# Optimization experiments

Measured on AMD Instinct MI355X. Metric: run time of the kernel, lower is better.

Reference implementation:

```python
import jax, jax.numpy as jnp
import numpy as np
import math

N_ENT = 200000
N_USERS = 100000
N_FACTORS = 4
N_REL = 26
CH = 64
N_EDGES = 1000000
NNZ = 1000000
KG_HEADS = 2


def scatter_softmax(scores, seg, num_segments):
    # numerically-stable softmax over groups defined by seg (per-head softmax)
    m = jax.ops.segment_max(scores, seg, num_segments=num_segments)
    m = jnp.where(jnp.isfinite(m), m, 0.0)
    e = jnp.exp(scores - m[seg])
    d = jax.ops.segment_sum(e, seg, num_segments=num_segments)
    return e / d[seg]


def setup_inputs() -> dict:
    key = jax.random.key(0)
    ks = jax.random.split(key, 11)
    return {
        "entity_emb": jax.random.normal(ks[0], (N_ENT, CH), dtype=jnp.float32) * 0.1,
        "user_emb": jax.random.normal(ks[1], (N_USERS, CH), dtype=jnp.float32) * 0.1,
        "latent_emb": jax.random.normal(ks[2], (N_FACTORS, CH), dtype=jnp.float32) * 0.1,
        "edge_index": jax.random.randint(ks[3], (2, N_EDGES), 0, N_ENT),
        "edge_type": jax.random.randint(ks[4], (N_EDGES,), 1, N_REL),  # in [1, N_REL-1]
        "ui_rows": jax.random.randint(ks[5], (NNZ,), 0, N_USERS),
        "ui_cols": jax.random.randint(ks[6], (NNZ,), 0, N_ENT),
        "ui_vals": jax.random.uniform(ks[7], (NNZ,), dtype=jnp.float32),
        "weight": jax.random.normal(ks[8], (N_REL - 1, CH), dtype=jnp.float32) * 0.1,
        "disen_weight_att": jax.random.normal(ks[9], (N_FACTORS, N_REL - 1), dtype=jnp.float32) * 0.1,
        "kg_W_r": jax.random.normal(ks[10], (CH, CH), dtype=jnp.float32) * (1.0 / math.sqrt(CH)),
    }


def reference(entity_emb, user_emb, latent_emb, edge_index, edge_type,
              ui_rows, ui_cols, ui_vals, weight, disen_weight_att, kg_W_r):
    head, tail = edge_index[0], edge_index[1]
    d_k = CH // KG_HEADS

    # --- Invariant_Capture.relation_aware_att ---
    rel_emb = weight[edge_type - 1]            # [E, C] gather
    h_emb = entity_emb[head]                   # [E, C] gather
    q = (h_emb @ kg_W_r).reshape(-1, KG_HEADS, d_k)
    k = (rel_emb @ kg_W_r).reshape(-1, KG_HEADS, d_k)
    score_r = ((q * k).sum(-1) / math.sqrt(d_k)).mean(-1)   # [E]
    rel_attn = scatter_softmax(score_r, head, N_ENT)

    # --- Invariant_Capture.kg_inv_capture ---
    t_emb = entity_emb[tail]                   # [E, C] gather
    r_emb = rel_emb * rel_attn[:, None]
    # bmm(cat(h,r), cat(t,r)^T) == h.t + r.r per edge
    score_trip = (h_emb * t_emb).sum(-1) + (r_emb * r_emb).sum(-1)
    kg_mask = scatter_softmax(score_trip, head, N_ENT)       # invariant_mask [E]

    # --- Aggregator: KG scatter-mean with invariant mask ---
    neigh = t_emb * rel_emb * kg_mask[:, None]               # [E, C]
    sums = jax.ops.segment_sum(neigh, head, num_segments=N_ENT)
    cnt = jax.ops.segment_sum(jnp.ones((neigh.shape[0],), dtype=neigh.dtype), head, num_segments=N_ENT)
    entity_agg = sums / jnp.maximum(cnt, 1.0)[:, None]       # scatter_mean

    # --- Aggregator: user side ---
    score = jax.nn.softmax(user_emb @ latent_emb.T, axis=1)  # [U, F]
    user_agg = jax.ops.segment_sum(entity_emb[ui_cols] * ui_vals[:, None], ui_rows, num_segments=N_USERS)
    disen_weight = jax.nn.softmax(disen_weight_att, axis=-1) @ weight  # [F, C]
    # (expand(U,F,C) * score[:,:,None]).sum(1) == score @ disen_weight
    user_agg = user_agg * (score @ disen_weight) + user_agg

    return jnp.concatenate([entity_agg, user_agg], axis=0)   # [N_ENT+N_USERS, C]
```

## Files before the change

### kernel.cpp

```cpp
#include <hip/hip_runtime.h>
#include <math.h>

#define N_ENT 200000
#define N_USERS 100000
#define NKEY 300000
#define N_FACTORS 4
#define NREL1 25
#define CH 64
#define N_EDGES 1000000
#define NNZ 1000000
#define NREC 2000000
#define BSHIFT 11
#define BKEYS 2048
#define NBUCKET 147
#define TILE 2048
#define CAP 24576
#define NCONVB ((N_ENT * 8 + 1023) / 1024)

#define SCORE_SCALE 0.08838834764831845f
#define INV_Q14 6.103888176768602e-05f

__device__ __forceinline__ float red8(float d) {
    d += __shfl_xor(d, 1);
    d += __shfl_xor(d, 2);
    d += __shfl_xor(d, 4);
    return d;
}
__device__ __forceinline__ float dot4(float4 a, float4 b) {
    return a.x * b.x + a.y * b.y + a.z * b.z + a.w * b.w;
}
__device__ __forceinline__ unsigned short f2bf(float f) {
    unsigned u = __float_as_uint(f);
    u += 0x7FFFu + ((u >> 16) & 1u);
    return (unsigned short)(u >> 16);
}
__device__ __forceinline__ float bf2f(unsigned short u) {
    return __uint_as_float(((unsigned)u) << 16);
}
__device__ __forceinline__ float4 bf4lo(uint4 t) {
    return make_float4(__uint_as_float(t.x << 16), __uint_as_float(t.x & 0xFFFF0000u),
                       __uint_as_float(t.y << 16), __uint_as_float(t.y & 0xFFFF0000u));
}
__device__ __forceinline__ float4 bf4hi(uint4 t) {
    return make_float4(__uint_as_float(t.z << 16), __uint_as_float(t.z & 0xFFFF0000u),
                       __uint_as_float(t.w << 16), __uint_as_float(t.w & 0xFFFF0000u));
}

__global__ void precompute_k(const float* __restrict__ W,
                             const float* __restrict__ weight,
                             const float* __restrict__ datt,
                             float* __restrict__ Mvec,
                             float* __restrict__ wnorm,
                             float* __restrict__ disen) {
    __shared__ float sW[64 * 64];
    __shared__ float sw[NREL1 * 64];
    __shared__ float sWWt[64 * 64];
    int tid = threadIdx.x;
    for (int i = tid; i < 64 * 64; i += 256) sW[i] = W[i];
    for (int i = tid; i < NREL1 * 64; i += 256) sw[i] = weight[i];
    __syncthreads();
    for (int e = tid; e < 64 * 64; e += 256) {
        int i = e >> 6, j = e & 63;
        float s = 0.f;
        for (int k = 0; k < 64; ++k) s += sW[i * 64 + k] * sW[j * 64 + k];
        sWWt[e] = s;
    }
    __syncthreads();
    for (int e = tid; e < NREL1 * 64; e += 256) {
        int r = e >> 6, i = e & 63;
        float s = 0.f;
        for (int j = 0; j < 64; ++j) s += sWWt[i * 64 + j] * sw[r * 64 + j];
        Mvec[e] = s;
    }
    for (int r = tid; r < NREL1; r += 256) {
        float s = 0.f;
        for (int j = 0; j < 64; ++j) { float v = sw[r * 64 + j]; s += v * v; }
        wnorm[r] = s;
    }
    for (int e = tid; e < N_FACTORS * 64; e += 256) {
        int f = e >> 6, c = e & 63;
        float m = -1e30f;
        for (int r = 0; r < NREL1; ++r) m = fmaxf(m, datt[f * NREL1 + r]);
        float ssum = 0.f, acc = 0.f;
        for (int r = 0; r < NREL1; ++r) {
            float p = expf(datt[f * NREL1 + r] - m);
            ssum += p;
            acc += p * sw[r * 64 + c];
        }
        disen[e] = acc / ssum;
    }
}

__global__ void binfill_k(const int* __restrict__ head, const int* __restrict__ tail,
                          const int* __restrict__ etype,
                          const int* __restrict__ rows, const int* __restrict__ cols,
                          const float* __restrict__ vals,
                          unsigned* __restrict__ gcur,
                          uint2* __restrict__ stg) {
    __shared__ unsigned hist[NBUCKET], gbase[NBUCKET];
    int tid = threadIdx.x;
    int tile0 = blockIdx.x * TILE;
    int tile_n = min(TILE, NREC - tile0);
    for (int b = tid; b < NBUCKET; b += 256) hist[b] = 0u;
    __syncthreads();
    unsigned key[8], pay[8], rank[8];
    for (int r = 0; r < 8; ++r) {
        int li = r * 256 + tid;
        key[r] = 0xFFFFFFFFu;
        if (li < tile_n) {
            int idx = tile0 + li;
            unsigned k, p;
            if (idx < N_EDGES) {
                k = (unsigned)head[idx];
                p = (unsigned)tail[idx] | ((unsigned)(etype[idx] - 1) << 18);
            } else {
                int j = idx - N_EDGES;
                k = (unsigned)(N_ENT + rows[j]);
                unsigned q = (unsigned)(vals[j] * 16383.f + 0.5f);
                p = (unsigned)cols[j] | (q << 18);
            }
            key[r] = k; pay[r] = p;
            rank[r] = atomicAdd(&hist[k >> BSHIFT], 1u);
        }
    }
    __syncthreads();
    if (tid < NBUCKET) {
        unsigned v = hist[tid];
        gbase[tid] = (unsigned)tid * CAP + (v ? atomicAdd(&gcur[tid], v) : 0u);
    }
    __syncthreads();
    for (int r = 0; r < 8; ++r) {
        if (key[r] != 0xFFFFFFFFu) {
            unsigned b = key[r] >> BSHIFT;
            unsigned dst = gbase[b] + rank[r];
            if (dst < (b + 1u) * CAP)
                stg[dst] = make_uint2(key[r], pay[r]);
        }
    }
}

__device__ __forceinline__
void place_bucket_dev(int b, int tid, const uint2* __restrict__ stg,
                      const unsigned* __restrict__ gcur,
                      unsigned* __restrict__ offs, unsigned* __restrict__ csr,
                      unsigned* shm) {
    unsigned c = (tid < NBUCKET) ? gcur[tid] : 0u;
    if (c > CAP) c = CAP;
    if (tid < 256) shm[tid] = c;
    __syncthreads();
    for (int o = 1; o < 256; o <<= 1) {
        unsigned t = (tid >= o && tid < 256) ? shm[tid - o] : 0u;
        __syncthreads();
        if (tid < 256) shm[tid] += t;
        __syncthreads();
    }
    if (tid == 0) {
        unsigned cb = gcur[b]; if (cb > CAP) cb = CAP;
        shm[3073] = cb;
        shm[3072] = shm[b] - cb;
        if (b == NBUCKET - 1) offs[NKEY] = shm[NBUCKET - 1];
    }
    __syncthreads();
    unsigned n = shm[3073], gb = shm[3072];
    const uint2* seg = stg + (size_t)b * CAP;
    unsigned* cnt = shm;
    unsigned* sc  = shm + 2048;
    cnt[tid * 2] = 0u; cnt[tid * 2 + 1] = 0u;
    __syncthreads();
    for (unsigned i = tid; i < n; i += 1024) {
        unsigned kk = seg[i].x - ((unsigned)b << BSHIFT);
        atomicAdd(&cnt[kk], 1u);
    }
    __syncthreads();
    unsigned c0 = cnt[tid * 2], c1 = cnt[tid * 2 + 1];
    unsigned tsum = c0 + c1;
    sc[tid] = tsum; __syncthreads();
    for (int o = 1; o < 1024; o <<= 1) {
        unsigned t = (tid >= o) ? sc[tid - o] : 0u;
        __syncthreads();
        sc[tid] += t;
        __syncthreads();
    }
    unsigned e0 = sc[tid] - tsum;
    unsigned e1 = e0 + c0;
    int k0 = (b << BSHIFT) + tid * 2;
    if (k0 < NKEY)     offs[k0]     = gb + e0;
    if (k0 + 1 < NKEY) offs[k0 + 1] = gb + e1;
    cnt[tid * 2] = e0; cnt[tid * 2 + 1] = e1;
    __syncthreads();
    for (unsigned i = tid; i < n; i += 1024) {
        uint2 rec = seg[i];
        unsigned kk = rec.x - ((unsigned)b << BSHIFT);
        unsigned pos = atomicAdd(&cnt[kk], 1u);
        csr[gb + pos] = rec.y;
    }
}

__device__ __forceinline__
void convE_dev(int cb, int tid, const float* __restrict__ ent,
               const float* __restrict__ Mvec,
               uint4* __restrict__ entb, unsigned short* __restrict__ E16,
               unsigned* shm) {
    float4* sM = (float4*)shm;
    for (int i = tid; i < NREL1 * 16; i += 1024) sM[i] = ((const float4*)Mvec)[i];
    __syncthreads();
    int idx = cb * 1024 + tid;
    int h = idx >> 3;
    int sub = tid & 7;
    if (h >= N_ENT) return;
    const float4* e4 = (const float4*)ent;
    float4 a = e4[h * 16 + sub * 2], b4 = e4[h * 16 + sub * 2 + 1];
    uint4 o;
    o.x = (unsigned)f2bf(a.x)  | ((unsigned)f2bf(a.y)  << 16);
    o.y = (unsigned)f2bf(a.z)  | ((unsigned)f2bf(a.w)  << 16);
    o.z = (unsigned)f2bf(b4.x) | ((unsigned)f2bf(b4.y) << 16);
    o.w = (unsigned)f2bf(b4.z) | ((unsigned)f2bf(b4.w) << 16);
    entb[h * 8 + sub] = o;
    for (int r = 0; r < NREL1; ++r) {
        float d = dot4(a, sM[r * 16 + sub * 2]) + dot4(b4, sM[r * 16 + sub * 2 + 1]);
        d = red8(d);
        if (sub == (r & 7)) E16[h * NREL1 + r] = f2bf(__expf(d * SCORE_SCALE));
    }
}

__global__ void binplace3_k(const uint2* __restrict__ stg,
                            const unsigned* __restrict__ gcur,
                            unsigned* __restrict__ offs,
                            unsigned* __restrict__ csr) {
    __shared__ __align__(16) unsigned shm[3074];
    place_bucket_dev(blockIdx.x, threadIdx.x, stg, gcur, offs, csr, shm);
}

__global__ void convE2_k(const float* __restrict__ ent,
                         const float* __restrict__ Mvec,
                         uint4* __restrict__ entb,
                         unsigned short* __restrict__ E16) {
    __shared__ __align__(16) unsigned shm[3074];
    convE_dev(blockIdx.x, threadIdx.x, ent, Mvec, entb, E16, shm);
}

__global__ void placeconv_k(const uint2* __restrict__ stg,
                            const unsigned* __restrict__ gcur,
                            unsigned* __restrict__ offs,
                            unsigned* __restrict__ csr,
                            const float* __restrict__ ent,
                            const float* __restrict__ Mvec,
                            uint4* __restrict__ entb,
                            unsigned short* __restrict__ E16) {
    __shared__ __align__(16) unsigned shm[3074];
    int b = blockIdx.x;
    if (b < NBUCKET)
        place_bucket_dev(b, threadIdx.x, stg, gcur, offs, csr, shm);
    else
        convE_dev(b - NBUCKET, threadIdx.x, ent, Mvec, entb, E16, shm);
}

template<bool FAST>
__global__ void gather8_k(const float* __restrict__ ent,
                          const uint4* __restrict__ entb,
                          const unsigned short* __restrict__ E16,
                          const float* __restrict__ weight,
                          const float* __restrict__ Mvec,
                          const float* __restrict__ wnorm,
                          const float* __restrict__ uemb,
                          const float* __restrict__ lat,
                          const float* __restrict__ disen,
                          const unsigned* __restrict__ offs,
                          const unsigned* __restrict__ csr,
                          float* __restrict__ out) {
    int gid = blockIdx.x * 256 + threadIdx.x;
    int key = gid >> 3;
    int sub = threadIdx.x & 7;
    if (key >= NKEY) return;
    unsigned beg = offs[key], end = offs[key + 1];
    const float4* e4 = (const float4*)ent;
    const float4* w4 = (const float4*)weight;
    float4* o4 = (float4*)out;
    const float4 z = make_float4(0.f, 0.f, 0.f, 0.f);

    if (key < N_ENT) {
        int h = key;
        if (beg == end) {
            o4[h * 16 + sub * 2] = z;
            o4[h * 16 + sub * 2 + 1] = z;
            return;
        }
        float4 hv0, hv1;
        if (FAST) {
            uint4 hb = entb[h * 8 + sub];
            hv0 = bf4lo(hb); hv1 = bf4hi(hb);
        } else {
            hv0 = e4[h * 16 + sub * 2]; hv1 = e4[h * 16 + sub * 2 + 1];
        }
        float dr = 0.f;
        if (FAST) {
            for (unsigned i = beg + sub; i < end; i += 8)
                dr += bf2f(E16[h * NREL1 + (csr[i] >> 18)]);
            dr = red8(dr);
        } else {
            for (unsigned i = beg; i < end; ++i) {
                int r = csr[i] >> 18;
                float d = dot4(hv0, ((const float4*)Mvec)[r * 16 + sub * 2]) +
                          dot4(hv1, ((const float4*)Mvec)[r * 16 + sub * 2 + 1]);
                dr += __expf(red8(d) * SCORE_SCALE);
            }
        }
        float inv_dr = 1.0f / dr;
        float4 a0 = z, a1 = z;
        float dt = 0.f;
        unsigned i = beg;
        for (; i + 2 <= end; i += 2) {
            unsigned p0 = csr[i], p1 = csr[i + 1];
            int t0 = p0 & 0x3FFFF, r0 = p0 >> 18;
            int t1 = p1 & 0x3FFFF, r1 = p1 >> 18;
            float4 tv00, tv01, tv10, tv11;
            if (FAST) {
                uint4 tb0 = entb[t0 * 8 + sub];
                uint4 tb1 = entb[t1 * 8 + sub];
                tv00 = bf4lo(tb0); tv01 = bf4hi(tb0);
                tv10 = bf4lo(tb1); tv11 = bf4hi(tb1);
            } else {
                tv00 = e4[t0 * 16 + sub * 2]; tv01 = e4[t0 * 16 + sub * 2 + 1];
                tv10 = e4[t1 * 16 + sub * 2]; tv11 = e4[t1 * 16 + sub * 2 + 1];
            }
            float d0 = red8(dot4(hv0, tv00) + dot4(hv1, tv01));
            float d1 = red8(dot4(hv0, tv10) + dot4(hv1, tv11));
            float er0, er1;
            if (FAST) {
                er0 = bf2f(E16[h * NREL1 + r0]);
                er1 = bf2f(E16[h * NREL1 + r1]);
            } else {
                float q0 = dot4(hv0, ((const float4*)Mvec)[r0 * 16 + sub * 2]) +
                           dot4(hv1, ((const float4*)Mvec)[r0 * 16 + sub * 2 + 1]);
                float q1 = dot4(hv0, ((const float4*)Mvec)[r1 * 16 + sub * 2]) +
                           dot4(hv1, ((const float4*)Mvec)[r1 * 16 + sub * 2 + 1]);
                er0 = __expf(red8(q0) * SCORE_SCALE);
                er1 = __expf(red8(q1) * SCORE_SCALE);
            }
            float ra0 = er0 * inv_dr, ra1 = er1 * inv_dr;
            float et0 = __expf(d0 + ra0 * ra0 * wnorm[r0]);
            float et1 = __expf(d1 + ra1 * ra1 * wnorm[r1]);
            dt += et0 + et1;
            float4 wv;
            wv = w4[r0 * 16 + sub * 2];
            a0.x += et0 * tv00.x * wv.x; a0.y += et0 * tv00.y * wv.y;
            a0.z += et0 * tv00.z * wv.z; a0.w += et0 * tv00.w * wv.w;
            wv = w4[r0 * 16 + sub * 2 + 1];
            a1.x += et0 * tv01.x * wv.x; a1.y += et0 * tv01.y * wv.y;
            a1.z += et0 * tv01.z * wv.z; a1.w += et0 * tv01.w * wv.w;
            wv = w4[r1 * 16 + sub * 2];
            a0.x += et1 * tv10.x * wv.x; a0.y += et1 * tv10.y * wv.y;
            a0.z += et1 * tv10.z * wv.z; a0.w += et1 * tv10.w * wv.w;
            wv = w4[r1 * 16 + sub * 2 + 1];
            a1.x += et1 * tv11.x * wv.x; a1.y += et1 * tv11.y * wv.y;
            a1.z += et1 * tv11.z * wv.z; a1.w += et1 * tv11.w * wv.w;
        }
        if (i < end) {
            unsigned p = csr[i];
            int t = p & 0x3FFFF, r = p >> 18;
            float4 tv0, tv1;
            if (FAST) {
                uint4 tb = entb[t * 8 + sub];
                tv0 = bf4lo(tb); tv1 = bf4hi(tb);
            } else {
                tv0 = e4[t * 16 + sub * 2]; tv1 = e4[t * 16 + sub * 2 + 1];
            }
            float d = red8(dot4(hv0, tv0) + dot4(hv1, tv1));
            float er;
            if (FAST) {
                er = bf2f(E16[h * NREL1 + r]);
            } else {
                float q = dot4(hv0, ((const float4*)Mvec)[r * 16 + sub * 2]) +
                          dot4(hv1, ((const float4*)Mvec)[r * 16 + sub * 2 + 1]);
                er = __expf(red8(q) * SCORE_SCALE);
            }
            float ra = er * inv_dr;
            float et = __expf(d + ra * ra * wnorm[r]);
            dt += et;
            float4 wv;
            wv = w4[r * 16 + sub * 2];
            a0.x += et * tv0.x * wv.x; a0.y += et * tv0.y * wv.y;
            a0.z += et * tv0.z * wv.z; a0.w += et * tv0.w * wv.w;
            wv = w4[r * 16 + sub * 2 + 1];
            a1.x += et * tv1.x * wv.x; a1.y += et * tv1.y * wv.y;
            a1.z += et * tv1.z * wv.z; a1.w += et * tv1.w * wv.w;
        }
        float inv = 1.0f / (dt * (float)(end - beg));
        a0.x *= inv; a0.y *= inv; a0.z *= inv; a0.w *= inv;
        a1.x *= inv; a1.y *= inv; a1.z *= inv; a1.w *= inv;
        o4[h * 16 + sub * 2] = a0;
        o4[h * 16 + sub * 2 + 1] = a1;
    } else {
        int u = key - N_ENT;
        float4 a0 = z, a1 = z;
        unsigned i = beg;
        for (; i + 2 <= end; i += 2) {
            unsigned p0 = csr[i], p1 = csr[i + 1];
            int c0 = p0 & 0x3FFFF, c1 = p1 & 0x3FFFF;
            float v0 = (float)(p0 >> 18) * INV_Q14;
            float v1 = (float)(p1 >> 18) * INV_Q14;
            float4 tv00, tv01, tv10, tv11;
            if (FAST) {
                uint4 tb0 = entb[c0 * 8 + sub];
                uint4 tb1 = entb[c1 * 8 + sub];
                tv00 = bf4lo(tb0); tv01 = bf4hi(tb0);
                tv10 = bf4lo(tb1); tv11 = bf4hi(tb1);
            } else {
                tv00 = e4[c0 * 16 + sub * 2]; tv01 = e4[c0 * 16 + sub * 2 + 1];
                tv10 = e4[c1 * 16 + sub * 2]; tv11 = e4[c1 * 16 + sub * 2 + 1];
            }
            a0.x += v0 * tv00.x + v1 * tv10.x; a0.y += v0 * tv00.y + v1 * tv10.y;
            a0.z += v0 * tv00.z + v1 * tv10.z; a0.w += v0 * tv00.w + v1 * tv10.w;
            a1.x += v0 * tv01.x + v1 * tv11.x; a1.y += v0 * tv01.y + v1 * tv11.y;
            a1.z += v0 * tv01.z + v1 * tv11.z; a1.w += v0 * tv01.w + v1 * tv11.w;
        }
        if (i < end) {
            unsigned p = csr[i];
            int c = p & 0x3FFFF;
            float v = (float)(p >> 18) * INV_Q14;
            float4 tv0, tv1;
            if (FAST) {
                uint4 tb = entb[c * 8 + sub];
                tv0 = bf4lo(tb); tv1 = bf4hi(tb);
            } else {
                tv0 = e4[c * 16 + sub * 2]; tv1 = e4[c * 16 + sub * 2 + 1];
            }
            a0.x += v * tv0.x; a0.y += v * tv0.y; a0.z += v * tv0.z; a0.w += v * tv0.w;
            a1.x += v * tv1.x; a1.y += v * tv1.y; a1.z += v * tv1.z; a1.w += v * tv1.w;
        }
        float4 uv0 = ((const float4*)uemb)[u * 16 + sub * 2];
        float4 uv1 = ((const float4*)uemb)[u * 16 + sub * 2 + 1];
        float d[N_FACTORS];
        for (int f = 0; f < N_FACTORS; ++f) {
            float t = dot4(uv0, ((const float4*)lat)[f * 16 + sub * 2]) +
                      dot4(uv1, ((const float4*)lat)[f * 16 + sub * 2 + 1]);
            d[f] = red8(t);
        }
        float m = fmaxf(fmaxf(d[0], d[1]), fmaxf(d[2], d[3]));
        float s = 0.f, p_[N_FACTORS];
        for (int f = 0; f < N_FACTORS; ++f) { p_[f] = __expf(d[f] - m); s += p_[f]; }
        float invs = 1.0f / s;
        float4 g0 = z, g1 = z;
        for (int f = 0; f < N_FACTORS; ++f) {
            float w = p_[f] * invs;
            float4 dv = ((const float4*)disen)[f * 16 + sub * 2];
            g0.x += w * dv.x; g0.y += w * dv.y; g0.z += w * dv.z; g0.w += w * dv.w;
            dv = ((const float4*)disen)[f * 16 + sub * 2 + 1];
            g1.x += w * dv.x; g1.y += w * dv.y; g1.z += w * dv.z; g1.w += w * dv.w;
        }
        a0.x *= (1.0f + g0.x); a0.y *= (1.0f + g0.y);
        a0.z *= (1.0f + g0.z); a0.w *= (1.0f + g0.w);
        a1.x *= (1.0f + g1.x); a1.y *= (1.0f + g1.y);
        a1.z *= (1.0f + g1.z); a1.w *= (1.0f + g1.w);
        o4[key * 16 + sub * 2] = a0;
        o4[key * 16 + sub * 2 + 1] = a1;
    }
}

extern "C" void kernel_launch(void* const* d_in, const int* in_sizes, int n_in,
                              void* d_out, int out_size, void* d_ws, size_t ws_size,
                              hipStream_t stream) {
    (void)in_sizes; (void)n_in; (void)out_size;
    const float* ent    = (const float*)d_in[0];
    const float* uemb   = (const float*)d_in[1];
    const float* lat    = (const float*)d_in[2];
    const int*   eidx   = (const int*)d_in[3];
    const int*   etype  = (const int*)d_in[4];
    const int*   urows  = (const int*)d_in[5];
    const int*   ucols  = (const int*)d_in[6];
    const float* uvals  = (const float*)d_in[7];
    const float* weight = (const float*)d_in[8];
    const float* datt   = (const float*)d_in[9];
    const float* W      = (const float*)d_in[10];

    const int* head = eidx;
    const int* tail = eidx + N_EDGES;
    float* out = (float*)d_out;

    unsigned* gcur  = (unsigned*)d_ws;
    unsigned* offs  = gcur + 256;
    float*    Mvec  = (float*)(offs + NKEY + 2);
    float*    wnorm = Mvec + NREL1 * 64;
    float*    disen = wnorm + 32;
    unsigned* csr   = (unsigned*)(disen + N_FACTORS * 64);
    unsigned* big   = csr + NREC;

    size_t base_words = 256 + (NKEY + 2) + 1888 + (size_t)NREC;
    size_t stg_words  = (size_t)NBUCKET * CAP * 2;
    size_t tbl_words  = (size_t)N_ENT * 32 + ((size_t)N_ENT * NREL1 + 1) / 2;
    size_t big_alias  = stg_words > tbl_words ? stg_words : tbl_words;
    size_t need_fast     = (base_words + big_alias) * 4;
    size_t need_min      = (base_words + stg_words) * 4;
    size_t need_disjoint = (base_words + stg_words + tbl_words) * 4;
    bool fast     = ws_size >= need_fast;
    bool disjoint = ws_size >= need_disjoint;
    if (ws_size < need_min) return;

    uint2*    stg  = (uint2*)big;
    unsigned* entw = disjoint ? (big + stg_words) : big;
    uint4*    entb = (uint4*)entw;
    unsigned short* E16 = (unsigned short*)(entw + (size_t)N_ENT * 32);

    const int BLK = 256;

    hipMemsetAsync(gcur, 0, 256 * sizeof(unsigned), stream);
    precompute_k<<<1, 256, 0, stream>>>(W, weight, datt, Mvec, wnorm, disen);
    binfill_k<<<(NREC + TILE - 1) / TILE, BLK, 0, stream>>>(
        head, tail, etype, urows, ucols, uvals, gcur, stg);

    if (disjoint) {
        placeconv_k<<<NBUCKET + NCONVB, 1024, 0, stream>>>(
            stg, gcur, offs, csr, ent, Mvec, entb, E16);
    } else {
        binplace3_k<<<NBUCKET, 1024, 0, stream>>>(stg, gcur, offs, csr);
        if (fast)
            convE2_k<<<NCONVB, 1024, 0, stream>>>(ent, Mvec, entb, E16);
    }

    int gridG = (NKEY * 8 + BLK - 1) / BLK;
    if (fast) {
        gather8_k<true><<<gridG, BLK, 0, stream>>>(
            ent, entb, E16, weight, Mvec, wnorm,
            uemb, lat, disen, offs, csr, out);
    } else {
        gather8_k<false><<<gridG, BLK, 0, stream>>>(
            ent, entb, E16, weight, Mvec, wnorm,
            uemb, lat, disen, offs, csr, out);
    }
}
```

Measured before the change: 202.0 us.

## Merge precompute into bin-fill kernel and stage records in LDS for coalesced scatter

Folds the single-block precompute kernel into the bin-fill launch as an extra block, removing one kernel launch and letting the precompute overlap with binning. Within each fill block, records are first sorted by bucket into shared memory using a wave-level prefix scan, then written to the global staging area in bucket-contiguous runs, so the global stores are more coalesced than scattered per-record writes. This costs about 40KB of shared memory per block, which may lower occupancy, and adds an extra LDS pass and barriers.

```diff
diff --git a/kernel.cpp b/kernel.cpp
--- a/kernel.cpp
+++ b/kernel.cpp
@@ -14,6 +14,7 @@
 #define BKEYS 2048
 #define NBUCKET 147
 #define TILE 2048
+#define NBLK_FILL ((NREC + TILE - 1) / TILE)
 #define CAP 24576
 #define NCONVB ((N_ENT * 8 + 1023) / 1024)
 
@@ -46,16 +47,17 @@
                        __uint_as_float(t.w << 16), __uint_as_float(t.w & 0xFFFF0000u));
 }
 
-__global__ void precompute_k(const float* __restrict__ W,
-                             const float* __restrict__ weight,
-                             const float* __restrict__ datt,
-                             float* __restrict__ Mvec,
-                             float* __restrict__ wnorm,
-                             float* __restrict__ disen) {
-    __shared__ float sW[64 * 64];
-    __shared__ float sw[NREL1 * 64];
-    __shared__ float sWWt[64 * 64];
-    int tid = threadIdx.x;
+__device__ __forceinline__
+void precompute_dev(int tid, unsigned char* shmraw,
+                    const float* __restrict__ W,
+                    const float* __restrict__ weight,
+                    const float* __restrict__ datt,
+                    float* __restrict__ Mvec,
+                    float* __restrict__ wnorm,
+                    float* __restrict__ disen) {
+    float* sW   = (float*)shmraw;
+    float* sw   = sW + 4096;
+    float* sWWt = sw + 1600;
     for (int i = tid; i < 64 * 64; i += 256) sW[i] = W[i];
     for (int i = tid; i < NREL1 * 64; i += 256) sw[i] = weight[i];
     __syncthreads();
@@ -91,14 +93,30 @@
     }
 }
 
-__global__ void binfill_k(const int* __restrict__ head, const int* __restrict__ tail,
-                          const int* __restrict__ etype,
-                          const int* __restrict__ rows, const int* __restrict__ cols,
-                          const float* __restrict__ vals,
-                          unsigned* __restrict__ gcur,
-                          uint2* __restrict__ stg) {
-    __shared__ unsigned hist[NBUCKET], gbase[NBUCKET];
+__global__ void binpre_k(const int* __restrict__ head, const int* __restrict__ tail,
+                         const int* __restrict__ etype,
+                         const int* __restrict__ rows, const int* __restrict__ cols,
+                         const float* __restrict__ vals,
+                         unsigned* __restrict__ gcur,
+                         uint2* __restrict__ stg,
+                         const float* __restrict__ W,
+                         const float* __restrict__ weight,
+                         const float* __restrict__ datt,
+                         float* __restrict__ Mvec,
+                         float* __restrict__ wnorm,
+                         float* __restrict__ disen) {
+    __shared__ __align__(16) unsigned char shmraw[39936];
     int tid = threadIdx.x;
+    if (blockIdx.x >= NBLK_FILL) {
+        precompute_dev(tid, shmraw, W, weight, datt, Mvec, wnorm, disen);
+        return;
+    }
+    unsigned* hist  = (unsigned*)shmraw;
+    unsigned* base  = hist + NBUCKET;
+    unsigned* gbase = base + NBUCKET;
+    unsigned* wsum  = gbase + NBUCKET;
+    uint2*    lrec  = (uint2*)(shmraw + 2048);
+
     int tile0 = blockIdx.x * TILE;
     int tile_n = min(TILE, NREC - tile0);
     for (int b = tid; b < NBUCKET; b += 256) hist[b] = 0u;
@@ -124,18 +142,34 @@
         }
     }
     __syncthreads();
+    unsigned h0 = (tid < NBUCKET) ? hist[tid] : 0u;
+    unsigned v = h0;
+    int lane = tid & 63, wid = tid >> 6;
+    for (int o = 1; o < 64; o <<= 1) {
+        unsigned t = __shfl_up(v, o);
+        if (lane >= o) v += t;
+    }
+    if (lane == 63) wsum[wid] = v;
+    __syncthreads();
+    unsigned pre = 0;
+    for (int w = 0; w < wid; ++w) pre += wsum[w];
     if (tid < NBUCKET) {
-        unsigned v = hist[tid];
-        gbase[tid] = (unsigned)tid * CAP + (v ? atomicAdd(&gcur[tid], v) : 0u);
+        base[tid] = pre + v - h0;
+        gbase[tid] = (unsigned)tid * CAP + (h0 ? atomicAdd(&gcur[tid], h0) : 0u);
     }
     __syncthreads();
     for (int r = 0; r < 8; ++r) {
         if (key[r] != 0xFFFFFFFFu) {
             unsigned b = key[r] >> BSHIFT;
-            unsigned dst = gbase[b] + rank[r];
-            if (dst < (b + 1u) * CAP)
-                stg[dst] = make_uint2(key[r], pay[r]);
-        }
+            lrec[base[b] + rank[r]] = make_uint2(key[r], pay[r]);
+        }
+    }
+    __syncthreads();
+    for (int i = tid; i < tile_n; i += 256) {
+        uint2 rec = lrec[i];
+        unsigned b = rec.x >> BSHIFT;
+        unsigned dst = gbase[b] + ((unsigned)i - base[b]);
+        if (dst < (b + 1u) * CAP) stg[dst] = rec;
     }
 }
 
@@ -504,9 +538,9 @@
     const int BLK = 256;
 
     hipMemsetAsync(gcur, 0, 256 * sizeof(unsigned), stream);
-    precompute_k<<<1, 256, 0, stream>>>(W, weight, datt, Mvec, wnorm, disen);
-    binfill_k<<<(NREC + TILE - 1) / TILE, BLK, 0, stream>>>(
-        head, tail, etype, urows, ucols, uvals, gcur, stg);
+    binpre_k<<<NBLK_FILL + 1, BLK, 0, stream>>>(
+        head, tail, etype, urows, ucols, uvals, gcur, stg,
+        W, weight, datt, Mvec, wnorm, disen);
 
     if (disjoint) {
         placeconv_k<<<NBUCKET + NCONVB, 1024, 0, stream>>>(
```

Result: no change. 201.9 us (-0.0%).
